# Performance work log

Hardware: AMD Instinct MI355X
Metric: run time of the kernel (lower is better)

## Reference

```python
import jax, jax.numpy as jnp
import numpy as np

N_NODES = 10000
N_EDGES = 160000
N_GRAPHS = 100
D = 32
E_DIM = 6
Q = 96
C = 2
EPS = 1e-5
S2S_STEPS = 3


def _bn(x, gamma, beta):
    # BatchNorm1d in training mode: normalize over the batch (row) axis
    mu = jnp.mean(x, axis=0)
    var = jnp.var(x, axis=0)
    return gamma * (x - mu) * jax.lax.rsqrt(var + EPS) + beta


def _mlp_layer(x, w, b, gamma, beta):
    # Linear -> ReLU -> BatchNorm1d (one block of the MLP helper)
    return _bn(jax.nn.relu(x @ w.T + b), gamma, beta)


def _nnconv(x, src, dst, edge_attr, nw, nb, ng, nbeta, root, bias):
    # edge MLP -> per-edge [D, D] weight matrices
    w = _mlp_layer(edge_attr, nw, nb, ng, nbeta).reshape(-1, D, D)  # [E, D, D]
    msg = jnp.einsum('ei,eio->eo', x[src], w)                       # per-edge matvec
    agg = jax.ops.segment_sum(msg, dst, num_segments=N_NODES)      # aggr='add'
    return agg + x @ root + bias                                    # root weight + bias


def _set2set(x, batch, w_ih, w_hh, b_ih, b_hh):
    h = jnp.zeros((N_GRAPHS, Q), x.dtype)
    c = jnp.zeros((N_GRAPHS, Q), x.dtype)
    q_star = jnp.zeros((N_GRAPHS, 2 * Q), x.dtype)
    for _ in range(S2S_STEPS):
        gates = q_star @ w_ih.T + b_ih + h @ w_hh.T + b_hh  # [B, 4Q], gate order i,f,g,o
        i, f, g, o = jnp.split(gates, 4, axis=1)
        c = jax.nn.sigmoid(f) * c + jax.nn.sigmoid(i) * jnp.tanh(g)
        h = jax.nn.sigmoid(o) * jnp.tanh(c)
        e = jnp.sum(x * h[batch], axis=-1)  # [N] attention logits
        emax = jax.ops.segment_max(e, batch, num_segments=N_GRAPHS)
        emax = jnp.where(jnp.isfinite(emax), emax, 0.0)
        a = jnp.exp(e - emax[batch])
        asum = jax.ops.segment_sum(a, batch, num_segments=N_GRAPHS)
        a = a / asum[batch]
        r = jax.ops.segment_sum(a[:, None] * x, batch, num_segments=N_GRAPHS)  # [B, Q]
        q_star = jnp.concatenate([h, r], axis=1)
    return q_star  # [B, 2Q]


def setup_inputs() -> dict:
    key = jax.random.key(0)
    ks = iter(jax.random.split(key, 48))
    def rn(shape, fan_in):
        return jax.random.normal(next(ks), shape, dtype=jnp.float32) * (1.0 / np.sqrt(fan_in))
    d = {}
    d['x'] = jax.random.normal(next(ks), (N_NODES, D), dtype=jnp.float32)
    d['edge_attr'] = jax.random.uniform(next(ks), (N_EDGES, E_DIM), dtype=jnp.float32)
    # conv1 edge-MLP + root + bias
    d['c1_nn_w'] = rn((D * D, E_DIM), E_DIM); d['c1_nn_b'] = jnp.zeros((D * D,), jnp.float32)
    d['c1_nn_g'] = jnp.ones((D * D,), jnp.float32); d['c1_nn_beta'] = jnp.zeros((D * D,), jnp.float32)
    d['c1_root'] = rn((D, D), D); d['c1_bias'] = jnp.zeros((D,), jnp.float32)
    # conv2
    d['c2_nn_w'] = rn((D * D, E_DIM), E_DIM); d['c2_nn_b'] = jnp.zeros((D * D,), jnp.float32)
    d['c2_nn_g'] = jnp.ones((D * D,), jnp.float32); d['c2_nn_beta'] = jnp.zeros((D * D,), jnp.float32)
    d['c2_root'] = rn((D, D), D); d['c2_bias'] = jnp.zeros((D,), jnp.float32)
    # lin1: MLP([2D, Q])
    d['lin1_w'] = rn((Q, 2 * D), 2 * D); d['lin1_b'] = jnp.zeros((Q,), jnp.float32)
    d['lin1_g'] = jnp.ones((Q,), jnp.float32); d['lin1_beta'] = jnp.zeros((Q,), jnp.float32)
    # Set2Set LSTM: input 2Q -> hidden Q
    d['lstm_w_ih'] = rn((4 * Q, 2 * Q), 2 * Q); d['lstm_w_hh'] = rn((4 * Q, Q), Q)
    d['lstm_b_ih'] = jnp.zeros((4 * Q,), jnp.float32); d['lstm_b_hh'] = jnp.zeros((4 * Q,), jnp.float32)
    # S2Slin: Linear(2Q, Q)
    d['s2s_w'] = rn((Q, 2 * Q), 2 * Q); d['s2s_b'] = jnp.zeros((Q,), jnp.float32)
    # mlp1: MLP([Q, Q, C])
    d['m1_w'] = rn((Q, Q), Q); d['m1_b'] = jnp.zeros((Q,), jnp.float32)
    d['m1_g'] = jnp.ones((Q,), jnp.float32); d['m1_beta'] = jnp.zeros((Q,), jnp.float32)
    d['m2_w'] = rn((C, Q), Q); d['m2_b'] = jnp.zeros((C,), jnp.float32)
    d['m2_g'] = jnp.ones((C,), jnp.float32); d['m2_beta'] = jnp.zeros((C,), jnp.float32)
    # graph structure
    d['edge_src'] = jax.random.randint(next(ks), (N_EDGES,), 0, N_NODES, dtype=jnp.int32)
    d['edge_dst'] = jax.random.randint(next(ks), (N_EDGES,), 0, N_NODES, dtype=jnp.int32)
    d['batch'] = jnp.sort(jax.random.randint(next(ks), (N_NODES,), 0, N_GRAPHS, dtype=jnp.int32))
    return d


def reference(x, edge_attr,
              c1_nn_w, c1_nn_b, c1_nn_g, c1_nn_beta, c1_root, c1_bias,
              c2_nn_w, c2_nn_b, c2_nn_g, c2_nn_beta, c2_root, c2_bias,
              lin1_w, lin1_b, lin1_g, lin1_beta,
              lstm_w_ih, lstm_w_hh, lstm_b_ih, lstm_b_hh,
              s2s_w, s2s_b,
              m1_w, m1_b, m1_g, m1_beta,
              m2_w, m2_b, m2_g, m2_beta,
              edge_src, edge_dst, batch):
    x1 = _nnconv(x, edge_src, edge_dst, edge_attr, c1_nn_w, c1_nn_b, c1_nn_g, c1_nn_beta, c1_root, c1_bias)
    x2 = _nnconv(x1, edge_src, edge_dst, edge_attr, c2_nn_w, c2_nn_b, c2_nn_g, c2_nn_beta, c2_root, c2_bias)
    xc = _mlp_layer(jnp.concatenate([x1, x2], axis=1), lin1_w, lin1_b, lin1_g, lin1_beta)  # [N, Q]
    qs = _set2set(xc, batch, lstm_w_ih, lstm_w_hh, lstm_b_ih, lstm_b_hh)                   # [B, 2Q]
    xg = qs @ s2s_w.T + s2s_b                                                               # [B, Q]
    xg = _mlp_layer(xg, m1_w, m1_b, m1_g, m1_beta)
    out = _mlp_layer(xg, m2_w, m2_b, m2_g, m2_beta)                                         # [B, C]
    return out
```

## Files before the change

kernel.cpp:

```cpp
#include <hip/hip_runtime.h>
#include <math.h>

#define NN 10000
#define NE 160000
#define NG 100
#define DD 32
#define QQ 96
#define EPS 1e-5f

__global__ __launch_bounds__(512) void k_stats4(const float* __restrict__ ea,
        const float* __restrict__ w1, const float* __restrict__ b1,
        const float* __restrict__ w2, const float* __restrict__ b2,
        float* __restrict__ stats) {
    __shared__ float eas[1536];
    const int tid = threadIdx.x;
    const int chunk = blockIdx.x >> 1;
    const int ct = ((blockIdx.x & 1) << 9) | tid;
    const float* wr1 = w1 + ct * 6;
    const float* wr2 = w2 + ct * 6;
    float2 W0 = make_float2(wr1[0], wr2[0]);
    float2 W1 = make_float2(wr1[1], wr2[1]);
    float2 W2 = make_float2(wr1[2], wr2[2]);
    float2 W3 = make_float2(wr1[3], wr2[3]);
    float2 W4 = make_float2(wr1[4], wr2[4]);
    float2 W5 = make_float2(wr1[5], wr2[5]);
    float2 Bb = make_float2(b1[ct], b2[ct]);
    float2 S = make_float2(0.f, 0.f), SS = make_float2(0.f, 0.f);
    const int base = chunk * 1536;
    eas[tid]        = ea[base + tid];
    eas[tid + 512]  = ea[base + tid + 512];
    eas[tid + 1024] = ea[base + tid + 1024];
    __syncthreads();
#pragma unroll 4
    for (int el = 0; el < 256; ++el) {
        const float* ep = &eas[el * 6];
        float2 p0 = *reinterpret_cast<const float2*>(ep);
        float2 p1 = *reinterpret_cast<const float2*>(ep + 2);
        float2 p2 = *reinterpret_cast<const float2*>(ep + 4);
        float2 y = Bb;
        y.x = fmaf(p0.x, W0.x, y.x); y.y = fmaf(p0.x, W0.y, y.y);
        y.x = fmaf(p0.y, W1.x, y.x); y.y = fmaf(p0.y, W1.y, y.y);
        y.x = fmaf(p1.x, W2.x, y.x); y.y = fmaf(p1.x, W2.y, y.y);
        y.x = fmaf(p1.y, W3.x, y.x); y.y = fmaf(p1.y, W3.y, y.y);
        y.x = fmaf(p2.x, W4.x, y.x); y.y = fmaf(p2.x, W4.y, y.y);
        y.x = fmaf(p2.y, W5.x, y.x); y.y = fmaf(p2.y, W5.y, y.y);
        float rx = fmaxf(y.x, 0.f), ry = fmaxf(y.y, 0.f);
        S.x += rx; S.y += ry;
        SS.x = fmaf(rx, rx, SS.x); SS.y = fmaf(ry, ry, SS.y);
    }
    atomicAdd(&stats[ct], S.x);
    atomicAdd(&stats[1024 + ct], SS.x);
    atomicAdd(&stats[2048 + ct], S.y);
    atomicAdd(&stats[3072 + ct], SS.y);
}

__global__ __launch_bounds__(256) void k_root(const float* __restrict__ x,
        const float* __restrict__ root, const float* __restrict__ bias,
        float* __restrict__ out,
        int doFin, const float* __restrict__ stats,
        const float* __restrict__ g1, const float* __restrict__ beta1,
        const float* __restrict__ g2, const float* __restrict__ beta2,
        const float* __restrict__ nw1, const float* __restrict__ nb1,
        const float* __restrict__ nw2, const float* __restrict__ nb2,
        float* __restrict__ wpack) {
    const int tid = threadIdx.x;
    if (doFin && blockIdx.x == gridDim.x - 1) {
        const float invE = 1.f / NE;
        for (int j = tid; j < 2048; j += 256) {
            int cv = j >> 10, col = j & 1023;
            const float* st = stats + cv * 2048;
            const float* g = cv ? g2 : g1;
            const float* bt = cv ? beta2 : beta1;
            const float* w = (cv ? nw2 : nw1) + col * 6;
            const float* nb = cv ? nb2 : nb1;
            float mean = st[col] * invE;
            float var = fmaxf(st[1024 + col] * invE - mean * mean, 0.f);
            float a = g[col] * rsqrtf(var + EPS);
            float b = bt[col] - mean * a;
            float* rec = wpack + cv * 12288 + col * 12;
            rec[0] = w[0]; rec[1] = w[1]; rec[2] = w[2];
            rec[3] = w[3]; rec[4] = w[4]; rec[5] = w[5];
            rec[6] = nb[col]; rec[7] = a; rec[8] = b;
        }
        return;
    }
    __shared__ float rlds[1024];
#pragma unroll
    for (int r = 0; r < 4; ++r) rlds[tid + 256 * r] = root[tid + 256 * r];
    __syncthreads();
    const int o = tid & 31;
    const int gg = tid >> 5;
    const int n = blockIdx.x * 8 + gg;
    if (n >= NN) return;
    const int half = tid & 32;
    float xs = x[n * 32 + o];
    float acc = bias[o];
#pragma unroll
    for (int i = 0; i < 32; ++i) {
        float xi = __shfl(xs, half | i);
        acc = fmaf(xi, rlds[i * 32 + o], acc);
    }
    out[n * 32 + o] = acc;
}

#define CACCP(PTR, XK, M) { \
    float4 _wa = *reinterpret_cast<const float4*>(PTR); \
    float4 _wb = *reinterpret_cast<const float4*>((PTR) + 4); \
    float _bv = (PTR)[8]; \
    float _y = _wb.z; \
    _y = fmaf(e0, _wa.x, _y); _y = fmaf(e1, _wa.y, _y); _y = fmaf(e2, _wa.z, _y); \
    _y = fmaf(e3, _wa.w, _y); _y = fmaf(e4, _wb.x, _y); _y = fmaf(e5, _wb.y, _y); \
    float _t = fmaf(_wb.w, fmaxf(_y, 0.f), _bv); M = fmaf(XK, _t, M); }

__global__ __launch_bounds__(256) void k_conv(const float* __restrict__ xin,
        const float* __restrict__ ea, const int* __restrict__ src, const int* __restrict__ dst,
        const float* __restrict__ wp, float* __restrict__ agg) {
    __shared__ float part[4][16][32];
    const int tid = threadIdx.x;
    const int lane = tid & 63;
    const int w = tid >> 6;
    const int p = lane >> 5;
    const int o = lane & 31;

    const float* r0 = wp + (((((w << 3) + 0 + p) << 5) | o) * 12);
    const float* r1 = wp + (((((w << 3) + 2 + p) << 5) | o) * 12);
    const float* r2 = wp + (((((w << 3) + 4 + p) << 5) | o) * 12);
    const float* r3 = wp + (((((w << 3) + 6 + p) << 5) | o) * 12);

    const int base0 = blockIdx.x * 80;
#pragma unroll 1
    for (int ch = 0; ch < 5; ++ch) {
        const int base = base0 + ch * 16;
#pragma unroll 4
        for (int m = 0; m < 16; ++m) {
            const int e = base + m;
            const int sc = src[e];
            const float* er = ea + e * 6;
            float e0 = er[0], e1 = er[1], e2 = er[2], e3 = er[3], e4 = er[4], e5 = er[5];
            const float* xr = xin + sc * 32 + (w << 3);
            float4 qa = *reinterpret_cast<const float4*>(xr);
            float4 qb = *reinterpret_cast<const float4*>(xr + 4);
            float xA = p ? qa.y : qa.x, xB = p ? qa.w : qa.z;
            float xC = p ? qb.y : qb.x, xD = p ? qb.w : qb.z;
            float msg = 0.f;
            CACCP(r0, xA, msg) CACCP(r1, xB, msg) CACCP(r2, xC, msg) CACCP(r3, xD, msg)
            msg += __shfl_xor(msg, 32, 64);
            if (p == 0) part[w][m][o] = msg;
        }
        __syncthreads();
        {
            const int m = tid >> 5;
            const int e = base + m;
            const int dd = dst[e];
            float sum = part[0][m][o] + part[1][m][o] + part[2][m][o] + part[3][m][o];
            atomicAdd(&agg[dd * 32 + o], sum);
            const int m2 = m + 8;
            const int e2 = base + m2;
            const int dd2 = dst[e2];
            float sum2 = part[0][m2][o] + part[1][m2][o] + part[2][m2][o] + part[3][m2][o];
            atomicAdd(&agg[dd2 * 32 + o], sum2);
        }
        __syncthreads();
    }
}

__global__ __launch_bounds__(384) void k_lin1a(const float* __restrict__ x1,
        const float* __restrict__ x2, const float* __restrict__ lw, const float* __restrict__ lb,
        float* __restrict__ pre, float* __restrict__ gsum, float* __restrict__ gsumsq) {
    __shared__ float cat[4][64];
    __shared__ float sh_s[96], sh_ss[96];
    const int tid = threadIdx.x;
    const int np = tid / 96;
    const int q = tid - np * 96;
    float w[64];
#pragma unroll
    for (int k = 0; k < 64; ++k) w[k] = lw[q * 64 + k];
    const float bq = lb[q];
    float s = 0.f, ss = 0.f;
    for (int nb = blockIdx.x * 4; nb < NN; nb += gridDim.x * 4) {
        __syncthreads();
        if (tid < 256) {
            int n2 = tid >> 6, k = tid & 63;
            cat[n2][k] = (k < 32) ? x1[(nb + n2) * 32 + k] : x2[(nb + n2) * 32 + (k - 32)];
        }
        __syncthreads();
        float v = bq;
#pragma unroll
        for (int k = 0; k < 64; ++k) v = fmaf(cat[np][k], w[k], v);
        float r = fmaxf(v, 0.f);
        pre[(nb + np) * 96 + q] = r;
        s += r; ss = fmaf(r, r, ss);
    }
    __syncthreads();
    if (tid < 96) { sh_s[tid] = 0.f; sh_ss[tid] = 0.f; }
    __syncthreads();
    atomicAdd(&sh_s[q], s);
    atomicAdd(&sh_ss[q], ss);
    __syncthreads();
    if (tid < 96) {
        atomicAdd(&gsum[tid], sh_s[tid]);
        atomicAdd(&gsumsq[tid], sh_ss[tid]);
    }
}

__global__ __launch_bounds__(512) void k_s2s(const float* __restrict__ pre,
        const int* __restrict__ batch,
        const float* __restrict__ gsum, const float* __restrict__ gsumsq,
        const float* __restrict__ lg, const float* __restrict__ lbeta,
        const float* __restrict__ w_ih, const float* __restrict__ w_hh,
        const float* __restrict__ b_ih, const float* __restrict__ b_hh,
        float* __restrict__ qs_g, float* __restrict__ e_ws) {
    __shared__ float qs[192], h[96], c[96], gates[384];
    __shared__ float ab_a[96], ab_b[96], hA[96], bh[96];
    __shared__ float redm[8], reds[8];
    __shared__ float racc_s[5][96];
    __shared__ float sh_scal[3];
    __shared__ int sse[2];
    const int tid = threadIdx.x;
    const int wid = tid >> 6, lane = tid & 63;
    const int b = blockIdx.x;
    if (tid < 2) {
        int key = b + tid, lo = 0, hi = NN;
        while (lo < hi) { int mid = (lo + hi) >> 1; if (batch[mid] < key) lo = mid + 1; else hi = mid; }
        sse[tid] = lo;
    }
    if (tid < 192) qs[tid] = 0.f;
    if (tid < 96) {
        h[tid] = 0.f; c[tid] = 0.f;
        const float invN = 1.f / NN;
        float mean = gsum[tid] * invN;
        float var = fmaxf(gsumsq[tid] * invN - mean * mean, 0.f);
        float a = lg[tid] * rsqrtf(var + EPS);
        ab_a[tid] = a;
        ab_b[tid] = lbeta[tid] - mean * a;
    }
    __syncthreads();
    const int s = sse[0], t = sse[1];
    for (int step = 0; step < 3; ++step) {
        if (tid < 384) {
            float acc = b_ih[tid] + b_hh[tid];
            const float* wi = &w_ih[tid * 192];
#pragma unroll 8
            for (int k = 0; k < 192; ++k) acc = fmaf(qs[k], wi[k], acc);
            const float* wh = &w_hh[tid * 96];
#pragma unroll 8
            for (int k = 0; k < 96; ++k) acc = fmaf(h[k], wh[k], acc);
            gates[tid] = acc;
        }
        __syncthreads();
        if (tid < 96) {
            float ig = 1.f / (1.f + __expf(-gates[tid]));
            float fg = 1.f / (1.f + __expf(-gates[96 + tid]));
            float gg = tanhf(gates[192 + tid]);
            float og = 1.f / (1.f + __expf(-gates[288 + tid]));
            float cn = fg * c[tid] + ig * gg;
            c[tid] = cn;
            float hn = og * tanhf(cn);
            h[tid] = hn;
            hA[tid] = ab_a[tid] * hn;
            bh[tid] = ab_b[tid] * hn;
        }
        __syncthreads();
        if (tid < 64) {
            float v = bh[tid] + (tid < 32 ? bh[64 + tid] : 0.f);
#pragma unroll
            for (int off = 32; off > 0; off >>= 1) v += __shfl_down(v, off);
            if (tid == 0) sh_scal[2] = v;
        }
        __syncthreads();
        const float hb = sh_scal[2];
        float pmax = -INFINITY;
        for (int n = s + tid; n < t; n += 512) {
            const float* xr = &pre[n * 96];
            float acc = hb;
#pragma unroll 8
            for (int k = 0; k < 96; ++k) acc = fmaf(xr[k], hA[k], acc);
            e_ws[n] = acc;
            pmax = fmaxf(pmax, acc);
        }
#pragma unroll
        for (int off = 32; off > 0; off >>= 1) pmax = fmaxf(pmax, __shfl_down(pmax, off));
        if (lane == 0) redm[wid] = pmax;
        __syncthreads();
        if (tid == 0) {
            float m = redm[0];
#pragma unroll
            for (int i = 1; i < 8; ++i) m = fmaxf(m, redm[i]);
            if (!isfinite(m)) m = 0.f;
            sh_scal[0] = m;
        }
        __syncthreads();
        const float emax = sh_scal[0];
        float pa = 0.f;
        for (int n = s + tid; n < t; n += 512) {
            float a = __expf(e_ws[n] - emax);
            e_ws[n] = a;
            pa += a;
        }
#pragma unroll
        for (int off = 32; off > 0; off >>= 1) pa += __shfl_down(pa, off);
        if (lane == 0) reds[wid] = pa;
        __syncthreads();
        if (tid == 0) {
            float a2 = 0.f;
#pragma unroll
            for (int i = 0; i < 8; ++i) a2 += reds[i];
            sh_scal[1] = (a2 > 0.f) ? 1.f / a2 : 0.f;
        }
        __syncthreads();
        const int g = tid / 96, q = tid - g * 96;
        if (tid < 480) {
            float racc = 0.f;
            for (int n = s + g; n < t; n += 5)
                racc = fmaf(e_ws[n], pre[n * 96 + q], racc);
            racc_s[g][q] = racc;
        }
        __syncthreads();
        if (tid < 96) {
            float inv = sh_scal[1];
            float racc5 = racc_s[0][tid] + racc_s[1][tid] + racc_s[2][tid]
                        + racc_s[3][tid] + racc_s[4][tid];
            float rq = (inv > 0.f) ? fmaf(ab_a[tid], racc5 * inv, ab_b[tid]) : 0.f;
            qs[tid] = h[tid];
            qs[96 + tid] = rq;
        }
        __syncthreads();
    }
    if (tid < 192) qs_g[b * 192 + tid] = qs[tid];
}

__global__ __launch_bounds__(128) void k_xg(const float* __restrict__ qs_g,
        const float* __restrict__ sw, const float* __restrict__ sb,
        const float* __restrict__ m1w, const float* __restrict__ m1b,
        float* __restrict__ pre, float* __restrict__ gsum, float* __restrict__ gsumsq) {
    __shared__ float xg0[96];
    const int tid = threadIdx.x;
    const int b = blockIdx.x;
    if (tid < 96) {
        const float* q = &qs_g[b * 192];
        float acc = sb[tid];
        const float* w = &sw[tid * 192];
#pragma unroll 8
        for (int k = 0; k < 192; ++k) acc = fmaf(q[k], w[k], acc);
        xg0[tid] = acc;
    }
    __syncthreads();
    if (tid < 96) {
        float acc = m1b[tid];
        const float* w = &m1w[tid * 96];
#pragma unroll 8
        for (int k = 0; k < 96; ++k) acc = fmaf(xg0[k], w[k], acc);
        float r = fmaxf(acc, 0.f);
        pre[b * 96 + tid] = r;
        atomicAdd(&gsum[tid], r);
        atomicAdd(&gsumsq[tid], r * r);
    }
}

__global__ __launch_bounds__(256) void k_tail(const float* __restrict__ pre,
        const float* __restrict__ gsum, const float* __restrict__ gsumsq,
        const float* __restrict__ g1, const float* __restrict__ beta1,
        const float* __restrict__ m2w, const float* __restrict__ m2b,
        const float* __restrict__ g2, const float* __restrict__ beta2,
        float* __restrict__ out) {
    __shared__ float xg1[100][97];
    __shared__ float pre2[200];
    __shared__ float ab2[4];
    const int tid = threadIdx.x;
    if (tid < 96) {
        const float invN = 1.f / NG;
        float mean = gsum[tid] * invN;
        float var = fmaxf(gsumsq[tid] * invN - mean * mean, 0.f);
        float a = g1[tid] * rsqrtf(var + EPS);
        float bb = beta1[tid] - mean * a;
        for (int n = 0; n < NG; ++n)
            xg1[n][tid] = fmaf(a, pre[n * 96 + tid], bb);
    }
    __syncthreads();
    if (tid < 200) {
        int n = tid >> 1, cc = tid & 1;
        float acc = m2b[cc];
        const float* w = &m2w[cc * 96];
#pragma unroll 8
        for (int k = 0; k < 96; ++k) acc = fmaf(xg1[n][k], w[k], acc);
        pre2[tid] = fmaxf(acc, 0.f);
    }
    __syncthreads();
    if (tid < 2) {
        float s = 0.f, ss = 0.f;
        for (int n = 0; n < NG; ++n) { float v = pre2[n * 2 + tid]; s += v; ss = fmaf(v, v, ss); }
        const float invN = 1.f / NG;
        float mean = s * invN;
        float var = fmaxf(ss * invN - mean * mean, 0.f);
        float a = g2[tid] * rsqrtf(var + EPS);
        ab2[tid] = a;
        ab2[2 + tid] = beta2[tid] - mean * a;
    }
    __syncthreads();
    if (tid < 200) {
        int cc = tid & 1;
        out[tid] = fmaf(ab2[cc], pre2[tid], ab2[2 + cc]);
    }
}

extern "C" void kernel_launch(void* const* d_in, const int* in_sizes, int n_in,
                              void* d_out, int out_size, void* d_ws, size_t ws_size,
                              hipStream_t stream) {
    (void)in_sizes; (void)n_in; (void)out_size; (void)ws_size;
    const float* x       = (const float*)d_in[0];
    const float* ea      = (const float*)d_in[1];
    const float* c1w     = (const float*)d_in[2];
    const float* c1b     = (const float*)d_in[3];
    const float* c1g     = (const float*)d_in[4];
    const float* c1beta  = (const float*)d_in[5];
    const float* c1root  = (const float*)d_in[6];
    const float* c1bias  = (const float*)d_in[7];
    const float* c2w     = (const float*)d_in[8];
    const float* c2b     = (const float*)d_in[9];
    const float* c2g     = (const float*)d_in[10];
    const float* c2beta  = (const float*)d_in[11];
    const float* c2root  = (const float*)d_in[12];
    const float* c2bias  = (const float*)d_in[13];
    const float* lin1w   = (const float*)d_in[14];
    const float* lin1b   = (const float*)d_in[15];
    const float* lin1g   = (const float*)d_in[16];
    const float* lin1bt  = (const float*)d_in[17];
    const float* wih     = (const float*)d_in[18];
    const float* whh     = (const float*)d_in[19];
    const float* bih     = (const float*)d_in[20];
    const float* bhh     = (const float*)d_in[21];
    const float* s2sw    = (const float*)d_in[22];
    const float* s2sb    = (const float*)d_in[23];
    const float* m1w     = (const float*)d_in[24];
    const float* m1b     = (const float*)d_in[25];
    const float* m1g     = (const float*)d_in[26];
    const float* m1beta  = (const float*)d_in[27];
    const float* m2w     = (const float*)d_in[28];
    const float* m2b     = (const float*)d_in[29];
    const float* m2g     = (const float*)d_in[30];
    const float* m2beta  = (const float*)d_in[31];
    const int* src       = (const int*)d_in[32];
    const int* dst       = (const int*)d_in[33];
    const int* batch     = (const int*)d_in[34];

    float* ws = (float*)d_ws;
    float* stats  = ws;
    float* AB     = ws + 4096;
    float* linst  = ws + 8192;
    float* m1st   = ws + 8384;
    float* wpack  = ws + 8704;
    float* x1     = wpack + 24576;
    float* x2     = x1 + 320000;
    float* prelin = x2 + 320000;
    float* e_ws   = prelin + 960000;
    float* qs_g   = e_ws + 10000;
    float* prem1  = qs_g + 19200;
    (void)AB;

    hipMemsetAsync(ws, 0, 8576 * sizeof(float), stream);

    k_stats4<<<1250, 512, 0, stream>>>(ea, c1w, c1b, c2w, c2b, stats);

    k_root<<<1251, 256, 0, stream>>>(x, c1root, c1bias, x1,
                                     1, stats, c1g, c1beta, c2g, c2beta,
                                     c1w, c1b, c2w, c2b, wpack);
    k_conv<<<2000, 256, 0, stream>>>(x, ea, src, dst, wpack, x1);

    k_root<<<1250, 256, 0, stream>>>(x1, c2root, c2bias, x2,
                                     0, stats, c1g, c1beta, c2g, c2beta,
                                     c1w, c1b, c2w, c2b, wpack);
    k_conv<<<2000, 256, 0, stream>>>(x1, ea, src, dst, wpack + 12288, x2);

    k_lin1a<<<500, 384, 0, stream>>>(x1, x2, lin1w, lin1b, prelin, linst, linst + 96);

    k_s2s<<<100, 512, 0, stream>>>(prelin, batch, linst, linst + 96, lin1g, lin1bt,
                                   wih, whh, bih, bhh, qs_g, e_ws);

    k_xg<<<100, 128, 0, stream>>>(qs_g, s2sw, s2sb, m1w, m1b, prem1, m1st, m1st + 96);
    k_tail<<<1, 256, 0, stream>>>(prem1, m1st, m1st + 96, m1g, m1beta,
                                  m2w, m2b, m2g, m2beta, (float*)d_out);
}
```

Measured before the change: 282.3 us.

## Widen conv blocks to 512 threads and keep per-edge weights in registers

```diff
diff --git a/kernel.cpp b/kernel.cpp
--- a/kernel.cpp
+++ b/kernel.cpp
@@ -8,7 +8,9 @@
 #define QQ 96
 #define EPS 1e-5f
 
-__global__ __launch_bounds__(512) void k_stats4(const float* __restrict__ ea,
+typedef float f2 __attribute__((ext_vector_type(2)));
+
+__global__ __launch_bounds__(512) void k_stats5(const float* __restrict__ ea,
         const float* __restrict__ w1, const float* __restrict__ b1,
         const float* __restrict__ w2, const float* __restrict__ b2,
         float* __restrict__ stats) {
@@ -18,14 +20,10 @@
     const int ct = ((blockIdx.x & 1) << 9) | tid;
     const float* wr1 = w1 + ct * 6;
     const float* wr2 = w2 + ct * 6;
-    float2 W0 = make_float2(wr1[0], wr2[0]);
-    float2 W1 = make_float2(wr1[1], wr2[1]);
-    float2 W2 = make_float2(wr1[2], wr2[2]);
-    float2 W3 = make_float2(wr1[3], wr2[3]);
-    float2 W4 = make_float2(wr1[4], wr2[4]);
-    float2 W5 = make_float2(wr1[5], wr2[5]);
-    float2 Bb = make_float2(b1[ct], b2[ct]);
-    float2 S = make_float2(0.f, 0.f), SS = make_float2(0.f, 0.f);
+    f2 W0 = {wr1[0], wr2[0]}, W1 = {wr1[1], wr2[1]}, W2 = {wr1[2], wr2[2]};
+    f2 W3 = {wr1[3], wr2[3]}, W4 = {wr1[4], wr2[4]}, W5 = {wr1[5], wr2[5]};
+    f2 Bb = {b1[ct], b2[ct]};
+    f2 S = {0.f, 0.f}, SS = {0.f, 0.f};
     const int base = chunk * 1536;
     eas[tid]        = ea[base + tid];
     eas[tid + 512]  = ea[base + tid + 512];
@@ -37,16 +35,16 @@
         float2 p0 = *reinterpret_cast<const float2*>(ep);
         float2 p1 = *reinterpret_cast<const float2*>(ep + 2);
         float2 p2 = *reinterpret_cast<const float2*>(ep + 4);
-        float2 y = Bb;
-        y.x = fmaf(p0.x, W0.x, y.x); y.y = fmaf(p0.x, W0.y, y.y);
-        y.x = fmaf(p0.y, W1.x, y.x); y.y = fmaf(p0.y, W1.y, y.y);
-        y.x = fmaf(p1.x, W2.x, y.x); y.y = fmaf(p1.x, W2.y, y.y);
-        y.x = fmaf(p1.y, W3.x, y.x); y.y = fmaf(p1.y, W3.y, y.y);
-        y.x = fmaf(p2.x, W4.x, y.x); y.y = fmaf(p2.x, W4.y, y.y);
-        y.x = fmaf(p2.y, W5.x, y.x); y.y = fmaf(p2.y, W5.y, y.y);
-        float rx = fmaxf(y.x, 0.f), ry = fmaxf(y.y, 0.f);
-        S.x += rx; S.y += ry;
-        SS.x = fmaf(rx, rx, SS.x); SS.y = fmaf(ry, ry, SS.y);
+        f2 y = Bb;
+        y = p0.x * W0 + y;
+        y = p0.y * W1 + y;
+        y = p1.x * W2 + y;
+        y = p1.y * W3 + y;
+        y = p2.x * W4 + y;
+        y = p2.y * W5 + y;
+        f2 r = {fmaxf(y.x, 0.f), fmaxf(y.y, 0.f)};
+        S = S + r;
+        SS = r * r + SS;
     }
     atomicAdd(&stats[ct], S.x);
     atomicAdd(&stats[1024 + ct], SS.x);
@@ -103,29 +101,34 @@
     out[n * 32 + o] = acc;
 }
 
-#define CACCP(PTR, XK, M) { \
-    float4 _wa = *reinterpret_cast<const float4*>(PTR); \
-    float4 _wb = *reinterpret_cast<const float4*>((PTR) + 4); \
-    float _bv = (PTR)[8]; \
-    float _y = _wb.z; \
-    _y = fmaf(e0, _wa.x, _y); _y = fmaf(e1, _wa.y, _y); _y = fmaf(e2, _wa.z, _y); \
-    _y = fmaf(e3, _wa.w, _y); _y = fmaf(e4, _wb.x, _y); _y = fmaf(e5, _wb.y, _y); \
-    float _t = fmaf(_wb.w, fmaxf(_y, 0.f), _bv); M = fmaf(XK, _t, M); }
-
-__global__ __launch_bounds__(256) void k_conv(const float* __restrict__ xin,
+#define CDECL(K) float w##K##0, w##K##1, w##K##2, w##K##3, w##K##4, w##K##5, bs##K, av##K, bv##K;
+#define CLOAD(K) { const int _j = (((w << 2) + (K << 1) + p) << 5) | o; \
+    const float* _r = wp + _j * 12; \
+    float4 _wa = *reinterpret_cast<const float4*>(_r); \
+    float4 _wb = *reinterpret_cast<const float4*>(_r + 4); \
+    w##K##0 = _wa.x; w##K##1 = _wa.y; w##K##2 = _wa.z; w##K##3 = _wa.w; \
+    w##K##4 = _wb.x; w##K##5 = _wb.y; bs##K = _wb.z; av##K = _wb.w; \
+    bv##K = _r[8]; }
+#define CPIN(K) asm("" : "+v"(w##K##0), "+v"(w##K##1), "+v"(w##K##2), "+v"(w##K##3), \
+                         "+v"(w##K##4), "+v"(w##K##5), "+v"(bs##K), "+v"(av##K), "+v"(bv##K));
+#define CACC(K, XK, M) { float _y = bs##K; \
+    _y = fmaf(e0, w##K##0, _y); _y = fmaf(e1, w##K##1, _y); _y = fmaf(e2, w##K##2, _y); \
+    _y = fmaf(e3, w##K##3, _y); _y = fmaf(e4, w##K##4, _y); _y = fmaf(e5, w##K##5, _y); \
+    float _t = fmaf(av##K, fmaxf(_y, 0.f), bv##K); M = fmaf(XK, _t, M); }
+
+__global__ __launch_bounds__(512) void k_conv(const float* __restrict__ xin,
         const float* __restrict__ ea, const int* __restrict__ src, const int* __restrict__ dst,
         const float* __restrict__ wp, float* __restrict__ agg) {
-    __shared__ float part[4][16][32];
+    __shared__ float part[8][16][32];
     const int tid = threadIdx.x;
     const int lane = tid & 63;
     const int w = tid >> 6;
     const int p = lane >> 5;
     const int o = lane & 31;
 
-    const float* r0 = wp + (((((w << 3) + 0 + p) << 5) | o) * 12);
-    const float* r1 = wp + (((((w << 3) + 2 + p) << 5) | o) * 12);
-    const float* r2 = wp + (((((w << 3) + 4 + p) << 5) | o) * 12);
-    const float* r3 = wp + (((((w << 3) + 6 + p) << 5) | o) * 12);
+    CDECL(0) CDECL(1)
+    CLOAD(0) CLOAD(1)
+    CPIN(0) CPIN(1)
 
     const int base0 = blockIdx.x * 80;
 #pragma unroll 1
@@ -137,13 +140,11 @@
             const int sc = src[e];
             const float* er = ea + e * 6;
             float e0 = er[0], e1 = er[1], e2 = er[2], e3 = er[3], e4 = er[4], e5 = er[5];
-            const float* xr = xin + sc * 32 + (w << 3);
-            float4 qa = *reinterpret_cast<const float4*>(xr);
-            float4 qb = *reinterpret_cast<const float4*>(xr + 4);
-            float xA = p ? qa.y : qa.x, xB = p ? qa.w : qa.z;
-            float xC = p ? qb.y : qb.x, xD = p ? qb.w : qb.z;
+            float4 qa = *reinterpret_cast<const float4*>(xin + sc * 32 + (w << 2));
+            float xA = p ? qa.y : qa.x;
+            float xB = p ? qa.w : qa.z;
             float msg = 0.f;
-            CACCP(r0, xA, msg) CACCP(r1, xB, msg) CACCP(r2, xC, msg) CACCP(r3, xD, msg)
+            CACC(0, xA, msg) CACC(1, xB, msg)
             msg += __shfl_xor(msg, 32, 64);
             if (p == 0) part[w][m][o] = msg;
         }
@@ -152,13 +153,9 @@
             const int m = tid >> 5;
             const int e = base + m;
             const int dd = dst[e];
-            float sum = part[0][m][o] + part[1][m][o] + part[2][m][o] + part[3][m][o];
+            float sum = part[0][m][o] + part[1][m][o] + part[2][m][o] + part[3][m][o]
+                      + part[4][m][o] + part[5][m][o] + part[6][m][o] + part[7][m][o];
             atomicAdd(&agg[dd * 32 + o], sum);
-            const int m2 = m + 8;
-            const int e2 = base + m2;
-            const int dd2 = dst[e2];
-            float sum2 = part[0][m2][o] + part[1][m2][o] + part[2][m2][o] + part[3][m2][o];
-            atomicAdd(&agg[dd2 * 32 + o], sum2);
         }
         __syncthreads();
     }
@@ -445,7 +442,6 @@
 
     float* ws = (float*)d_ws;
     float* stats  = ws;
-    float* AB     = ws + 4096;
     float* linst  = ws + 8192;
     float* m1st   = ws + 8384;
     float* wpack  = ws + 8704;
@@ -455,21 +451,20 @@
     float* e_ws   = prelin + 960000;
     float* qs_g   = e_ws + 10000;
     float* prem1  = qs_g + 19200;
-    (void)AB;
 
     hipMemsetAsync(ws, 0, 8576 * sizeof(float), stream);
 
-    k_stats4<<<1250, 512, 0, stream>>>(ea, c1w, c1b, c2w, c2b, stats);
+    k_stats5<<<1250, 512, 0, stream>>>(ea, c1w, c1b, c2w, c2b, stats);
 
     k_root<<<1251, 256, 0, stream>>>(x, c1root, c1bias, x1,
                                      1, stats, c1g, c1beta, c2g, c2beta,
                                      c1w, c1b, c2w, c2b, wpack);
-    k_conv<<<2000, 256, 0, stream>>>(x, ea, src, dst, wpack, x1);
+    k_conv<<<2000, 512, 0, stream>>>(x, ea, src, dst, wpack, x1);
 
     k_root<<<1250, 256, 0, stream>>>(x1, c2root, c2bias, x2,
                                      0, stats, c1g, c1beta, c2g, c2beta,
                                      c1w, c1b, c2w, c2b, wpack);
-    k_conv<<<2000, 256, 0, stream>>>(x1, ea, src, dst, wpack + 12288, x2);
+    k_conv<<<2000, 512, 0, stream>>>(x1, ea, src, dst, wpack + 12288, x2);
 
     k_lin1a<<<500, 384, 0, stream>>>(x1, x2, lin1w, lin1b, prelin, linst, linst + 96);
 
```

Result: slower. 318.6 us (+12.9%).
